# Optimization experiments

Hardware: AMD Instinct MI355X
Metric: run time of the kernel (lower is better)

Reference implementation:

```python
import jax, jax.numpy as jnp
import numpy as np

# Detector / geometry constants (mirrors DRR.__init__ kwargs)
SDD = 1020.0           # source-to-detector distance (mm)
H, W = 160, 160        # detector pixels
DELX, DELY = 2.5, 2.5  # pixel pitch (mm)
X0, Y0 = 0.0, 0.0
VOL = 256              # CT volume is VOL^3 voxels
SPACING = 1.5          # voxel spacing (mm)
EPS = 1e-8


def setup_inputs() -> dict:
    key = jax.random.key(0)
    density = jax.random.uniform(key, (VOL, VOL, VOL), dtype=jnp.float32)
    # rigid camera pose: rotate the C-arm about x; isocenter at the world origin
    th = 0.2
    c, s = np.cos(th), np.sin(th)
    R = np.array([[1, 0, 0], [0, c, -s], [0, s, c]], dtype=np.float32)
    t = R @ np.array([0.0, 0.0, -SDD / 2.0], dtype=np.float32)  # source 510mm from isocenter
    pose = np.eye(4, dtype=np.float32)
    pose[:3, :3], pose[:3, 3] = R, t
    # voxel -> world affine: isotropic spacing, volume centered at the origin
    affine = np.eye(4, dtype=np.float32)
    affine[:3, :3] *= SPACING
    affine[:3, 3] = -SPACING * VOL / 2.0
    affine_inv = jnp.asarray(np.linalg.inv(affine).astype(np.float32))
    return {"density": density, "pose": jnp.asarray(pose)[None], "affine_inv": affine_inv}


def _detector_rays():
    # camera frame: X-ray source at the origin, detector plane at z = SDD
    xs = (jnp.arange(W, dtype=jnp.float32) - (W - 1) / 2.0) * DELX + X0
    ys = (jnp.arange(H, dtype=jnp.float32) - (H - 1) / 2.0) * DELY + Y0
    tx, ty = jnp.meshgrid(xs, ys, indexing="xy")
    targets = jnp.stack([tx.ravel(), ty.ravel(), jnp.full((H * W,), SDD, jnp.float32)], -1)
    source = jnp.zeros((1, 3), jnp.float32)
    return source, targets  # [1,3], [H*W,3]


def _pose_apply(pose, pts):  # pose [B,4,4], pts [N,3] -> [B,N,3]
    return jnp.einsum("bij,nj->bni", pose[:, :3, :3], pts) + pose[:, None, :3, 3]


def _affine_apply(A, pts):  # A [4,4], pts [B,N,3] -> [B,N,3]
    return jnp.einsum("ij,bnj->bni", A[:3, :3], pts) + A[:3, 3]


def _siddon(density, src, tgt, raylen):
    # Exact Siddon line integral. src [B,1,3], tgt [B,N,3] in voxel coords.
    dims = jnp.asarray(density.shape, jnp.float32)
    sd = tgt - src                                   # ray directions [B,N,3]
    sd_safe = jnp.where(jnp.abs(sd) < EPS, EPS, sd)  # avoid div-by-zero
    # parametric entry/exit of the segment with the volume bounding box
    a0 = (0.0 - src) / sd_safe
    a1 = (dims - src) / sd_safe
    amin = jnp.maximum(jnp.max(jnp.minimum(a0, a1), -1), 0.0)  # [B,N]
    amax = jnp.minimum(jnp.min(jnp.maximum(a0, a1), -1), 1.0)
    amax = jnp.maximum(amax, amin)
    # intersections with every axis-aligned voxel plane, sorted per ray
    planes = [
        (jnp.arange(n + 1, dtype=jnp.float32)[None, None, :] - src[..., i:i + 1]) / sd_safe[..., i:i + 1]
        for i, n in enumerate(density.shape)
    ]
    alphas = jnp.sort(jnp.concatenate(planes, -1), -1)          # [B,N,P], P = sum(n_i+1)
    # clamping collapses out-of-volume intersections to zero-length intervals
    alphas = jnp.clip(alphas, amin[..., None], amax[..., None])
    steps = jnp.diff(alphas, axis=-1)                           # [B,N,P-1] segment lengths (in alpha)
    amid = 0.5 * (alphas[..., :-1] + alphas[..., 1:])           # segment midpoints
    # voxel index at each midpoint, computed per axis to avoid a [B,N,P,3] stack
    idx = tuple(
        jnp.clip(jnp.floor(src[..., i:i + 1] + amid * sd[..., i:i + 1]).astype(jnp.int32), 0, density.shape[i] - 1)
        for i in range(3)
    )
    vox = density[idx[0], idx[1], idx[2]]                       # irregular gather [B,N,P-1]
    return jnp.sum(vox * steps, -1) * raylen                    # [B,N]


def reference(density, pose, affine_inv):
    src_c, tgt_c = _detector_rays()
    src_w = _pose_apply(pose, src_c)                 # [B,1,3]
    tgt_w = _pose_apply(pose, tgt_c)                 # [B,N,3]
    raylen = jnp.linalg.norm(tgt_w - src_w, axis=-1)  # img = (target-source).norm(dim=-1)
    src_v = _affine_apply(affine_inv, src_w)          # world -> voxel
    tgt_v = _affine_apply(affine_inv, tgt_w)
    drr = _siddon(density, src_v, tgt_v, raylen)
    return drr.reshape(pose.shape[0], 1, H, W)        # img.view(len(pose), -1, H, W)
```

## Files before the change

### kernel.cpp

```cpp
#include <hip/hip_runtime.h>

static constexpr float F_SDD = 1020.0f;
static constexpr int   DH = 160, DW = 160;
static constexpr float DELX = 2.5f, DELY = 2.5f;
static constexpr int   VOL = 256;
static constexpr int   NRAY = DH * DW;
static constexpr int   TILES_X = DW / 8;
static constexpr int   TILES_Y = DH / 8;
static constexpr int   NTILE = TILES_X * TILES_Y;
static constexpr int   CHUNKS = 8;
static constexpr int   SUBS = 4;
static constexpr int   KB = 4;
static constexpr float EPS = 1e-8f;

extern "C" __global__ void zero_out_kernel(float* __restrict__ out, int n) {
    int i = blockIdx.x * blockDim.x + threadIdx.x;
    if (i < n) out[i] = 0.0f;
}

extern "C" __global__ void __launch_bounds__(256, 8)
drr_siddon_kernel(const float* __restrict__ density,
                  const float* __restrict__ pose,
                  const float* __restrict__ ainv,
                  float* __restrict__ out)
{
    __shared__ float red[256];

    int chunk = blockIdx.x & (CHUNKS - 1);
    int tile  = blockIdx.x >> 3;
    int tx = tile % TILES_X, ty = tile / TILES_X;

    int tid  = threadIdx.x;
    int sub  = tid >> 6;
    int lane = tid & 63;

    int px = tx * 8 + (lane & 7);
    int py = ty * 8 + (lane >> 3);
    int ray = py * DW + px;

    float xs = ((float)px - (DW - 1) * 0.5f) * DELX;
    float ys = ((float)py - (DH - 1) * 0.5f) * DELY;

    float R00 = pose[0], R01 = pose[1], R02 = pose[2],  t0 = pose[3];
    float R10 = pose[4], R11 = pose[5], R12 = pose[6],  t1 = pose[7];
    float R20 = pose[8], R21 = pose[9], R22 = pose[10], t2 = pose[11];

    float sw0 = t0, sw1 = t1, sw2 = t2;
    float tw0 = R00 * xs + R01 * ys + R02 * F_SDD + t0;
    float tw1 = R10 * xs + R11 * ys + R12 * F_SDD + t1;
    float tw2 = R20 * xs + R21 * ys + R22 * F_SDD + t2;

    float dw0 = tw0 - sw0, dw1 = tw1 - sw1, dw2 = tw2 - sw2;
    float raylen = sqrtf(dw0 * dw0 + dw1 * dw1 + dw2 * dw2);

    float A00 = ainv[0], A01 = ainv[1], A02 = ainv[2],  A03 = ainv[3];
    float A10 = ainv[4], A11 = ainv[5], A12 = ainv[6],  A13 = ainv[7];
    float A20 = ainv[8], A21 = ainv[9], A22 = ainv[10], A23 = ainv[11];

    float s0 = A00 * sw0 + A01 * sw1 + A02 * sw2 + A03;
    float s1 = A10 * sw0 + A11 * sw1 + A12 * sw2 + A13;
    float s2 = A20 * sw0 + A21 * sw1 + A22 * sw2 + A23;
    float g0 = A00 * tw0 + A01 * tw1 + A02 * tw2 + A03;
    float g1 = A10 * tw0 + A11 * tw1 + A12 * tw2 + A13;
    float g2 = A20 * tw0 + A21 * tw1 + A22 * tw2 + A23;

    float sd0 = g0 - s0, sd1 = g1 - s1, sd2 = g2 - s2;
    float e0 = (fabsf(sd0) < EPS) ? EPS : sd0;
    float e1 = (fabsf(sd1) < EPS) ? EPS : sd1;
    float e2 = (fabsf(sd2) < EPS) ? EPS : sd2;
    float inv0 = 1.0f / e0, inv1 = 1.0f / e1, inv2 = 1.0f / e2;

    float lo0 = (0.0f - s0) * inv0, hi0 = ((float)VOL - s0) * inv0;
    float lo1 = (0.0f - s1) * inv1, hi1 = ((float)VOL - s1) * inv1;
    float lo2 = (0.0f - s2) * inv2, hi2 = ((float)VOL - s2) * inv2;
    float amin = fmaxf(fmaxf(fminf(lo0, hi0), fminf(lo1, hi1)), fminf(lo2, hi2));
    amin = fmaxf(amin, 0.0f);
    float amax = fminf(fminf(fmaxf(lo0, hi0), fmaxf(lo1, hi1)), fmaxf(lo2, hi2));
    amax = fminf(amax, 1.0f);
    amax = fmaxf(amax, amin);

    float arange  = amax - amin;
    float c_start = amin + arange * ((float)chunk * (1.0f / CHUNKS));
    float c_end   = (chunk == CHUNKS - 1) ? amax
                    : amin + arange * ((float)(chunk + 1) * (1.0f / CHUNKS));
    float crange  = c_end - c_start;
    float a_start = c_start + crange * ((float)sub * (1.0f / SUBS));
    float a_end   = (sub == SUBS - 1) ? c_end
                    : c_start + crange * ((float)(sub + 1) * (1.0f / SUBS));

    float ax0, ax1, ax2, da0, da1, da2;
    if (fabsf(sd0) < EPS) { ax0 = 3.0e38f; da0 = 0.0f; }
    else {
        float p = s0 + a_start * sd0;
        float k = (sd0 > 0.0f) ? (floorf(p) + 1.0f) : (ceilf(p) - 1.0f);
        ax0 = (k - s0) * inv0; da0 = fabsf(inv0);
    }
    if (fabsf(sd1) < EPS) { ax1 = 3.0e38f; da1 = 0.0f; }
    else {
        float p = s1 + a_start * sd1;
        float k = (sd1 > 0.0f) ? (floorf(p) + 1.0f) : (ceilf(p) - 1.0f);
        ax1 = (k - s1) * inv1; da1 = fabsf(inv1);
    }
    if (fabsf(sd2) < EPS) { ax2 = 3.0e38f; da2 = 0.0f; }
    else {
        float p = s2 + a_start * sd2;
        float k = (sd2 > 0.0f) ? (floorf(p) + 1.0f) : (ceilf(p) - 1.0f);
        ax2 = (k - s2) * inv2; da2 = fabsf(inv2);
    }

    float acc = 0.0f;
    float alpha = a_start;
    float4 quad = make_float4(0.f, 0.f, 0.f, 0.f);
    int qbase = -8;
    while (alpha < a_end) {
        float  seg[KB];
        int    dsel[KB];
        bool   miss[KB];
        float4 ld[KB];
#pragma unroll
        for (int k = 0; k < KB; ++k) {
            float m     = fminf(fminf(ax0, ax1), ax2);
            float astop = fminf(m, a_end);
            float amid  = 0.5f * (alpha + astop);
            seg[k] = fmaxf(astop - alpha, 0.0f);
            float c0 = truncf(fminf(fmaxf(fmaf(amid, sd0, s0), 0.0f), 255.0f));
            float c1 = truncf(fminf(fmaxf(fmaf(amid, sd1, s1), 0.0f), 255.0f));
            float c2 = truncf(fminf(fmaxf(fmaf(amid, sd2, s2), 0.0f), 255.0f));
            int idx = (int)fmaf(c0, 65536.0f, fmaf(c1, 256.0f, c2));
            int d = idx - qbase;
            miss[k] = ((unsigned)d >= 4u);
            if (miss[k]) {
                qbase = idx & ~3;
                ld[k] = *(const float4*)(density + qbase);
                d = idx - qbase;
            }
            dsel[k] = d;
            if (ax0 <= m) ax0 += da0;
            if (ax1 <= m) ax1 += da1;
            if (ax2 <= m) ax2 += da2;
            alpha = m;
        }
#pragma unroll
        for (int k = 0; k < KB; ++k) {
            if (miss[k]) quad = ld[k];
            int d = dsel[k];
            float v = (d & 2) ? ((d & 1) ? quad.w : quad.z)
                              : ((d & 1) ? quad.y : quad.x);
            acc = fmaf(v, seg[k], acc);
        }
    }

    red[tid] = acc;
    __syncthreads();
    if (tid < 64) {
        float total = red[tid] + red[tid + 64] + red[tid + 128] + red[tid + 192];
        atomicAdd(&out[ray], total * raylen);
    }
}

extern "C" void kernel_launch(void* const* d_in, const int* in_sizes, int n_in,
                              void* d_out, int out_size, void* d_ws, size_t ws_size,
                              hipStream_t stream) {
    const float* density = (const float*)d_in[0];
    const float* pose    = (const float*)d_in[1];
    const float* ainv    = (const float*)d_in[2];
    float* out = (float*)d_out;

    hipLaunchKernelGGL(zero_out_kernel, dim3((NRAY + 255) / 256), dim3(256), 0,
                       stream, out, NRAY);

    dim3 block(256);
    dim3 grid(NTILE * CHUNKS);
    hipLaunchKernelGGL(drr_siddon_kernel, grid, block, 0, stream,
                       density, pose, ainv, out);
}
```

Measured before the change: 28.79 us.

## Precompute per-ray setup in a separate kernel and double sub-splits per block

Moves the per-ray geometry (pose and affine transforms, reciprocals, entry/exit alphas, ray length) into a setup kernel that also zeroes the output and writes the values to workspace. The main Siddon kernel reads them back instead of recomputing them in every one of the chunk blocks. The block grows to 512 threads with 8 sub-segments per ray, doubling the parallel traversal work per ray. In exchange the main kernel does extra global reads, the launch-bounds occupancy hint (512, 8) may not be achievable, and the per-thread segments become shorter.

New measurement: 35.68 us. 23.9% more time.

```diff
diff --git a/kernel.cpp b/kernel.cpp
--- a/kernel.cpp
+++ b/kernel.cpp
@@ -9,34 +9,21 @@
 static constexpr int   TILES_Y = DH / 8;
 static constexpr int   NTILE = TILES_X * TILES_Y;
 static constexpr int   CHUNKS = 8;
-static constexpr int   SUBS = 4;
+static constexpr int   SUBS = 8;
 static constexpr int   KB = 4;
 static constexpr float EPS = 1e-8f;
 
-extern "C" __global__ void zero_out_kernel(float* __restrict__ out, int n) {
-    int i = blockIdx.x * blockDim.x + threadIdx.x;
-    if (i < n) out[i] = 0.0f;
-}
 
-extern "C" __global__ void __launch_bounds__(256, 8)
-drr_siddon_kernel(const float* __restrict__ density,
-                  const float* __restrict__ pose,
-                  const float* __restrict__ ainv,
-                  float* __restrict__ out)
+extern "C" __global__ void __launch_bounds__(256)
+drr_setup_kernel(const float* __restrict__ pose,
+                 const float* __restrict__ ainv,
+                 float* __restrict__ W,
+                 float* __restrict__ out)
 {
-    __shared__ float red[256];
-
-    int chunk = blockIdx.x & (CHUNKS - 1);
-    int tile  = blockIdx.x >> 3;
-    int tx = tile % TILES_X, ty = tile / TILES_X;
-
-    int tid  = threadIdx.x;
-    int sub  = tid >> 6;
-    int lane = tid & 63;
-
-    int px = tx * 8 + (lane & 7);
-    int py = ty * 8 + (lane >> 3);
-    int ray = py * DW + px;
+    int ray = blockIdx.x * blockDim.x + threadIdx.x;
+    if (ray >= NRAY) return;
+    int py = ray / DW;
+    int px = ray - py * DW;
 
     float xs = ((float)px - (DW - 1) * 0.5f) * DELX;
     float ys = ((float)py - (DH - 1) * 0.5f) * DELY;
@@ -79,6 +66,39 @@
     amax = fminf(amax, 1.0f);
     amax = fmaxf(amax, amin);
 
+    W[ray            ] = s0;   W[ray +  1 * NRAY] = s1;  W[ray +  2 * NRAY] = s2;
+    W[ray +  3 * NRAY] = sd0;  W[ray +  4 * NRAY] = sd1; W[ray +  5 * NRAY] = sd2;
+    W[ray +  6 * NRAY] = inv0; W[ray +  7 * NRAY] = inv1;W[ray +  8 * NRAY] = inv2;
+    W[ray +  9 * NRAY] = amin; W[ray + 10 * NRAY] = amax;
+    W[ray + 11 * NRAY] = raylen;
+    out[ray] = 0.0f;
+}
+
+extern "C" __global__ void __launch_bounds__(512, 8)
+drr_siddon_kernel(const float* __restrict__ density,
+                  const float* __restrict__ W,
+                  float* __restrict__ out)
+{
+    __shared__ float red[512];
+
+    int chunk = blockIdx.x & (CHUNKS - 1);
+    int tile  = blockIdx.x >> 3;
+    int tx = tile % TILES_X, ty = tile / TILES_X;
+
+    int tid  = threadIdx.x;
+    int sub  = tid >> 6;
+    int lane = tid & 63;
+
+    int px = tx * 8 + (lane & 7);
+    int py = ty * 8 + (lane >> 3);
+    int ray = py * DW + px;
+
+    float s0   = W[ray            ], s1   = W[ray +  1 * NRAY], s2   = W[ray +  2 * NRAY];
+    float sd0  = W[ray +  3 * NRAY], sd1  = W[ray +  4 * NRAY], sd2  = W[ray +  5 * NRAY];
+    float inv0 = W[ray +  6 * NRAY], inv1 = W[ray +  7 * NRAY], inv2 = W[ray +  8 * NRAY];
+    float amin = W[ray +  9 * NRAY], amax = W[ray + 10 * NRAY];
+    float raylen = W[ray + 11 * NRAY];
+
     float arange  = amax - amin;
     float c_start = amin + arange * ((float)chunk * (1.0f / CHUNKS));
     float c_end   = (chunk == CHUNKS - 1) ? amax
@@ -88,25 +108,21 @@
     float a_end   = (sub == SUBS - 1) ? c_end
                     : c_start + crange * ((float)(sub + 1) * (1.0f / SUBS));
 
-    float ax0, ax1, ax2, da0, da1, da2;
-    if (fabsf(sd0) < EPS) { ax0 = 3.0e38f; da0 = 0.0f; }
-    else {
-        float p = s0 + a_start * sd0;
-        float k = (sd0 > 0.0f) ? (floorf(p) + 1.0f) : (ceilf(p) - 1.0f);
-        ax0 = (k - s0) * inv0; da0 = fabsf(inv0);
-    }
-    if (fabsf(sd1) < EPS) { ax1 = 3.0e38f; da1 = 0.0f; }
-    else {
-        float p = s1 + a_start * sd1;
-        float k = (sd1 > 0.0f) ? (floorf(p) + 1.0f) : (ceilf(p) - 1.0f);
-        ax1 = (k - s1) * inv1; da1 = fabsf(inv1);
-    }
-    if (fabsf(sd2) < EPS) { ax2 = 3.0e38f; da2 = 0.0f; }
-    else {
-        float p = s2 + a_start * sd2;
-        float k = (sd2 > 0.0f) ? (floorf(p) + 1.0f) : (ceilf(p) - 1.0f);
-        ax2 = (k - s2) * inv2; da2 = fabsf(inv2);
-    }
+    float da0 = fabsf(inv0), da1 = fabsf(inv1), da2 = fabsf(inv2);
+
+    float ax0, ax1, ax2;
+    if (fabsf(sd0) < EPS) ax0 = 3.0e38f;
+    else { float p = s0 + a_start * sd0;
+           float kk = (sd0 > 0.0f) ? (floorf(p) + 1.0f) : (ceilf(p) - 1.0f);
+           ax0 = (kk - s0) * inv0; }
+    if (fabsf(sd1) < EPS) ax1 = 3.0e38f;
+    else { float p = s1 + a_start * sd1;
+           float kk = (sd1 > 0.0f) ? (floorf(p) + 1.0f) : (ceilf(p) - 1.0f);
+           ax1 = (kk - s1) * inv1; }
+    if (fabsf(sd2) < EPS) ax2 = 3.0e38f;
+    else { float p = s2 + a_start * sd2;
+           float kk = (sd2 > 0.0f) ? (floorf(p) + 1.0f) : (ceilf(p) - 1.0f);
+           ax2 = (kk - s2) * inv2; }
 
     float acc = 0.0f;
     float alpha = a_start;
@@ -153,7 +169,9 @@
     red[tid] = acc;
     __syncthreads();
     if (tid < 64) {
-        float total = red[tid] + red[tid + 64] + red[tid + 128] + red[tid + 192];
+        float total = red[tid];
+#pragma unroll
+        for (int j = 1; j < SUBS; ++j) total += red[tid + j * 64];
         atomicAdd(&out[ray], total * raylen);
     }
 }
@@ -165,12 +183,13 @@
     const float* pose    = (const float*)d_in[1];
     const float* ainv    = (const float*)d_in[2];
     float* out = (float*)d_out;
+    float* W   = (float*)d_ws;
 
-    hipLaunchKernelGGL(zero_out_kernel, dim3((NRAY + 255) / 256), dim3(256), 0,
-                       stream, out, NRAY);
+    hipLaunchKernelGGL(drr_setup_kernel, dim3((NRAY + 255) / 256), dim3(256),
+                       0, stream, pose, ainv, W, out);
 
-    dim3 block(256);
+    dim3 block(512);
     dim3 grid(NTILE * CHUNKS);
     hipLaunchKernelGGL(drr_siddon_kernel, grid, block, 0, stream,
-                       density, pose, ainv, out);
+                       density, W, out);
 }
```
